# Kernel tuning notes

Measured on AMD Instinct MI355X. Metric: run time of the kernel, lower is better.

Reference implementation:

```python
import jax, jax.numpy as jnp
import numpy as np

K = 3
KK = K * K


def _offset_mask_conv(x, ow, ob):
    # Conv2d(C_in, 3*KK, k=3, stride=1, pad=1) in NCHW/OIHW
    y = jax.lax.conv_general_dilated(
        x, ow, window_strides=(1, 1), padding=((1, 1), (1, 1)),
        dimension_numbers=('NCHW', 'OIHW', 'NCHW'))
    return y + ob[None, :, None, None]


def _bilinear(xb, gy, gx):
    # xb: [C,H,W]; gy,gx: [KK,H,W] pixel coords (align_corners=True => pixel==unnormalized)
    # padding_mode='zeros': out-of-range taps contribute 0.
    C, H, W = xb.shape
    x0f = jnp.floor(gx); y0f = jnp.floor(gy)
    x0 = x0f.astype(jnp.int32); y0 = y0f.astype(jnp.int32)
    x1 = x0 + 1; y1 = y0 + 1
    wx1 = gx - x0f; wy1 = gy - y0f
    wx0 = 1.0 - wx1; wy0 = 1.0 - wy1

    def gather(yi, xi):
        valid = (yi >= 0) & (yi < H) & (xi >= 0) & (xi < W)
        yc = jnp.clip(yi, 0, H - 1)
        xc = jnp.clip(xi, 0, W - 1)
        v = xb[:, yc, xc]  # [C,KK,H,W]
        return v * valid[None].astype(xb.dtype)

    return (gather(y0, x0) * (wy0 * wx0)[None]
            + gather(y0, x1) * (wy0 * wx1)[None]
            + gather(y1, x0) * (wy1 * wx0)[None]
            + gather(y1, x1) * (wy1 * wx1)[None])  # [C,KK,H,W]


def setup_inputs() -> dict:
    key = jax.random.key(0)
    k1, k2, k3, k4 = jax.random.split(key, 4)
    B, C, Cout, H, W = 8, 64, 64, 128, 128
    x = jax.random.normal(k1, (B, C, H, W), dtype=jnp.float32)
    # offset/mask conv params (small, so offsets stay in a realistic range)
    ow = jax.random.normal(k2, (3 * KK, C, K, K), dtype=jnp.float32) * 0.01
    ob = jnp.zeros((3 * KK,), dtype=jnp.float32)
    # main conv weight (kaiming-ish scale) and bias
    w = jax.random.normal(k3, (Cout, C, K, K), dtype=jnp.float32) * (1.0 / np.sqrt(C * KK))
    b = jax.random.normal(k4, (Cout,), dtype=jnp.float32) * 0.01
    return {"x": x, "ow": ow, "ob": ob, "w": w, "b": b}


def reference(x, ow, ob, w, b):
    B, C, H, W = x.shape
    om = _offset_mask_conv(x, ow, ob)            # [B, 3*KK, H, W]
    off_x = om[:, :KK]                           # o1 -> x-offset
    off_y = om[:, KK:2 * KK]                     # o2 -> y-offset
    mask = jax.nn.sigmoid(om[:, 2 * KK:])        # [B,KK,H,W]

    gh, gw = jnp.meshgrid(jnp.arange(H, dtype=x.dtype), jnp.arange(W, dtype=x.dtype), indexing='ij')
    d = jnp.arange(-(K // 2), K // 2 + 1, dtype=x.dtype)
    kh, kw = jnp.meshgrid(d, d, indexing='ij')
    dh = kh.reshape(-1)                          # [KK] row-major (dh,dw) order matches weight[...,i,j]
    dw = kw.reshape(-1)

    gx = gw[None, None] + dw[None, :, None, None] + off_x   # [B,KK,H,W]
    gy = gh[None, None] + dh[None, :, None, None] + off_y

    sampled = jax.vmap(_bilinear)(x, gy, gx)     # [B,C,KK,H,W]
    sampled = sampled * mask[:, None]            # modulation

    wflat = w.reshape(w.shape[0], w.shape[1], KK)  # [Cout,C,KK]
    out = jnp.einsum('bckhw,ock->bohw', sampled, wflat) + b[None, :, None, None]
    return out
```

## Files before the change

### kernel.cpp

```cpp
#include <hip/hip_runtime.h>

#define B 8
#define C 64
#define H 128
#define W 128
#define HW (H * W)
#define OC 27
#define KK 9
#define COUT 64
#define KDIM 576
#define LDSROW 1152
#define NPIX 16
#define NPAIR (NPIX * KK)

typedef __attribute__((ext_vector_type(8))) short s16x8;
typedef __attribute__((ext_vector_type(4))) float f32x4;

__device__ inline ushort f2bf(float f) {
    union { float f; unsigned u; } uv;
    uv.f = f;
    unsigned r = uv.u + 0x7FFF + ((uv.u >> 16) & 1);
    return (ushort)(r >> 16);
}
__device__ inline float bf2f(ushort u) {
    return __uint_as_float((unsigned)u << 16);
}

__global__ __launch_bounds__(256) void k_transpose_x(const float* __restrict__ x,
                                                     ushort* __restrict__ xTb) {
    __shared__ float lds[64][65];
    int b = blockIdx.x >> 8;
    int tile = blockIdx.x & 255;
    int hw0 = tile * 64;
    int lane = threadIdx.x & 63;
    int cg = threadIdx.x >> 6;
#pragma unroll
    for (int r = 0; r < 16; ++r) {
        int c = cg * 16 + r;
        lds[c][lane] = x[(size_t)(b * C + c) * HW + hw0 + lane];
    }
    __syncthreads();
#pragma unroll
    for (int r = 0; r < 16; ++r) {
        int hwl = cg * 16 + r;
        xTb[(size_t)(b * HW + hw0 + hwl) * C + lane] = f2bf(lds[lane][hwl]);
    }
}

__global__ __launch_bounds__(256) void k_prep_w(const float* __restrict__ w,
                                                ushort* __restrict__ wB) {
    int idx = blockIdx.x * 256 + threadIdx.x;
    if (idx >= COUT * KDIM) return;
    int o = idx / KDIM;
    int Kx = idx % KDIM;
    int k = Kx >> 6;
    int c = Kx & 63;
    wB[idx] = f2bf(w[(size_t)(o * C + c) * KK + k]);
}

__global__ __launch_bounds__(256) void k_prep_aw(const float* __restrict__ ow,
                                                 ushort* __restrict__ awB) {
    int idx = blockIdx.x * 256 + threadIdx.x;
    if (idx >= 32 * KDIM) return;
    int o = idx / KDIM;
    int Kx = idx % KDIM;
    int tap = Kx >> 6;
    int c = Kx & 63;
    float v = (o < OC) ? ow[((size_t)o * C + c) * KK + tap] : 0.0f;
    awB[idx] = f2bf(v);
}

__global__ __launch_bounds__(256) void k_om(const ushort* __restrict__ xTb,
                                            const ushort* __restrict__ awB,
                                            const float* __restrict__ ob,
                                            float* __restrict__ om) {
    __shared__ __align__(16) char xwin[3 * 66 * 128];
    int tid = threadIdx.x;
    int lane = tid & 63;
    int wv = tid >> 6;
    int blk = blockIdx.x;
    int b = blk >> 8;
    int h = (blk >> 1) & 127;
    int w0 = (blk & 1) * 64;

    const ushort* xb = xTb + (size_t)b * (HW * C);
    int ch2 = tid & 31;
#pragma unroll
    for (int it = 0; it < 25; ++it) {
        int pi = it * 8 + (tid >> 5);
        if (pi < 198) {
            int row = pi / 66;
            int col = pi - row * 66;
            int y = h - 1 + row;
            int xc = w0 - 1 + col;
            unsigned v = 0;
            if ((unsigned)y < H && (unsigned)xc < W)
                v = *(const unsigned*)(xb + ((size_t)(y * W + xc) << 6) + ch2 * 2);
            int byte = (pi * 128 + ch2 * 4) ^ ((col & 7) << 4);
            *(unsigned*)(xwin + byte) = v;
        }
    }
    __syncthreads();

    f32x4 acc0 = {0.f, 0.f, 0.f, 0.f};
    f32x4 acc1 = {0.f, 0.f, 0.f, 0.f};
    int pixl = lane & 15;
    int q = lane >> 4;
    int base_col = wv * 16 + pixl;
    const ushort* a0 = awB + (size_t)pixl * KDIM + q * 8;
    const ushort* a1 = awB + (size_t)(16 + pixl) * KDIM + q * 8;
#pragma unroll
    for (int s = 0; s < 18; ++s) {
        int tap = s >> 1;
        int row = tap / 3;
        int cs = tap - row * 3;
        int col = base_col + cs;
        int c0b = ((s & 1) * 32 + q * 8) * 2;
        int byte = (((row * 66 + col) << 7) + c0b) ^ ((col & 7) << 4);
        s16x8 bfrag = *(const s16x8*)(xwin + byte);
        s16x8 af0 = *(const s16x8*)(a0 + s * 32);
        s16x8 af1 = *(const s16x8*)(a1 + s * 32);
        acc0 = __builtin_amdgcn_mfma_f32_16x16x32_bf16(af0, bfrag, acc0, 0, 0, 0);
        acc1 = __builtin_amdgcn_mfma_f32_16x16x32_bf16(af1, bfrag, acc1, 0, 0, 0);
    }

    int pix = wv * 16 + pixl;
#pragma unroll
    for (int j = 0; j < 4; ++j) {
        int oc = q * 4 + j;
        om[(((size_t)b * OC + oc) * H + h) * W + w0 + pix] = acc0[j] + ob[oc];
        int oc1 = 16 + q * 4 + j;
        if (oc1 < OC)
            om[(((size_t)b * OC + oc1) * H + h) * W + w0 + pix] = acc1[j] + ob[oc1];
    }
}

__global__ __launch_bounds__(256, 6) void k_main(const ushort* __restrict__ xTb,
                                                 const float* __restrict__ om,
                                                 const ushort* __restrict__ wB,
                                                 const float* __restrict__ bias,
                                                 float* __restrict__ out) {
    __shared__ __align__(16) char smem[NPIX * LDSROW];
    __shared__ float4 meta_w[NPAIR];
    __shared__ int2 meta_o[NPAIR];

    int tid = threadIdx.x;
    int lane = tid & 63;
    int wv = tid >> 6;
    int pb = blockIdx.x * NPIX;
    int b = pb >> 14;
    int rem = pb & (HW - 1);
    int h = rem >> 7;
    int w0 = rem & (W - 1);

    if (tid < NPAIR) {
        int k = tid >> 4;
        int p = tid & 15;
        int dh = k / 3 - 1;
        int dw = k % 3 - 1;
        const float* o0 = om + ((size_t)b * OC) * HW + h * W + w0 + p;
        float offx = o0[(size_t)k * HW];
        float offy = o0[(size_t)(KK + k) * HW];
        float mlog = o0[(size_t)(2 * KK + k) * HW];
        float mask = 1.0f / (1.0f + __expf(-mlog));
        float gx = (float)(w0 + p + dw) + offx;
        float gy = (float)(h + dh) + offy;
        float x0f = floorf(gx), y0f = floorf(gy);
        int x0 = (int)x0f, y0 = (int)y0f;
        int x1 = x0 + 1, y1 = y0 + 1;
        float wx1 = gx - x0f, wy1 = gy - y0f;
        float wx0 = 1.0f - wx1, wy0 = 1.0f - wy1;
        float rw0 = ((unsigned)y0 < H) ? wy0 * mask : 0.0f;
        float rw1 = ((unsigned)y1 < H) ? wy1 * mask : 0.0f;
        int y0c = min(max(y0, 0), H - 1), y1c = min(max(y1, 0), H - 1);
        int colbase = min(max(x0, 0), W - 2);
        float cw0 = 0.0f, cw1 = 0.0f;
        if ((unsigned)x0 < W) { if (x0 == colbase) cw0 += wx0; else cw1 += wx0; }
        if ((unsigned)x1 < W) { if (x1 == colbase) cw0 += wx1; else cw1 += wx1; }
        meta_w[tid] = make_float4(rw0 * cw0, rw0 * cw1, rw1 * cw0, rw1 * cw1);
        meta_o[tid] = make_int2((y0c * W + colbase) * (C * 2),
                                (y1c * W + colbase) * (C * 2));
    }
    __syncthreads();

    const char* xbase = (const char*)(xTb + (size_t)b * (HW * C));
#pragma unroll
    for (int pp = 0; pp < 4; ++pp) {
        int p = wv * 4 + pp;
        int vlds = p * LDSROW + ((lane * 2) ^ ((p & 7) << 4));
#pragma unroll
        for (int k = 0; k < KK; ++k) {
            int pair = k * 16 + p;
            float4 mw = meta_w[pair];
            int2 mo = meta_o[pair];
            const ushort* r0 =
                (const ushort*)(xbase + __builtin_amdgcn_readfirstlane(mo.x));
            const ushort* r1 =
                (const ushort*)(xbase + __builtin_amdgcn_readfirstlane(mo.y));
            float g00 = bf2f(r0[lane]);
            float g01 = bf2f(r0[64 + lane]);
            float g10 = bf2f(r1[lane]);
            float g11 = bf2f(r1[64 + lane]);
            float v = g00 * mw.x + g01 * mw.y + g10 * mw.z + g11 * mw.w;
            *(ushort*)(smem + vlds + k * 128) = f2bf(v);
        }
    }
    __syncthreads();

    f32x4 acc;
#pragma unroll
    for (int j = 0; j < 4; ++j) acc[j] = bias[wv * 16 + (lane >> 4) * 4 + j];

    int pix = lane & 15;
    const ushort* wrow = wB + (size_t)(wv * 16 + pix) * KDIM + (lane >> 4) * 8;
#pragma unroll
    for (int s = 0; s < 18; ++s) {
        int kbyte = s * 64 + (lane >> 4) * 16;
        int byte = (pix * LDSROW + kbyte) ^ ((pix & 7) << 4);
        s16x8 bfrag = *(const s16x8*)(smem + byte);
        s16x8 afrag = *(const s16x8*)(wrow + s * 32);
        acc = __builtin_amdgcn_mfma_f32_16x16x32_bf16(afrag, bfrag, acc, 0, 0, 0);
    }

    float* obase = out + ((size_t)(b * COUT + wv * 16 + (lane >> 4) * 4) * HW) + h * W + w0;
#pragma unroll
    for (int j = 0; j < 4; ++j) obase[(size_t)j * HW + pix] = acc[j];
}

extern "C" void kernel_launch(void* const* d_in, const int* in_sizes, int n_in,
                              void* d_out, int out_size, void* d_ws, size_t ws_size,
                              hipStream_t stream) {
    const float* x = (const float*)d_in[0];
    const float* ow = (const float*)d_in[1];
    const float* ob = (const float*)d_in[2];
    const float* w = (const float*)d_in[3];
    const float* bias = (const float*)d_in[4];
    float* out = (float*)d_out;

    float* om = (float*)d_ws;
    ushort* xTb = (ushort*)(om + (size_t)B * OC * HW);
    ushort* wB = xTb + (size_t)B * HW * C;
    ushort* awB = wB + (size_t)COUT * KDIM;

    hipLaunchKernelGGL(k_transpose_x, dim3(B * 256), dim3(256), 0, stream, x, xTb);
    hipLaunchKernelGGL(k_prep_w, dim3((COUT * KDIM + 255) / 256), dim3(256), 0,
                       stream, w, wB);
    hipLaunchKernelGGL(k_prep_aw, dim3((32 * KDIM + 255) / 256), dim3(256), 0,
                       stream, ow, awB);
    hipLaunchKernelGGL(k_om, dim3(B * H * 2), dim3(256), 0, stream, xTb, awB, ob, om);
    hipLaunchKernelGGL(k_main, dim3(B * HW / NPIX), dim3(256), 0, stream,
                       xTb, om, wB, bias, out);
}
```

Baseline: 172.0 us.

## Gather bilinear taps as packed bf16 pairs with cross-half shuffle reduction

The deformable sampling loop now loads 4-byte words (two bf16 channels) per lane instead of four separate 2-byte loads. The low half-wave handles the left column tap and the high half the right, and a 32-lane xor shuffle combines them. All 18 loads for a pixel are issued before any math to raise memory-level parallelism, and results are packed with the hardware bf16 convert. The aim is fewer, wider global loads and fewer instructions, at the cost of more registers, shuffle overhead, and half the lanes idling on the LDS store.

```diff
diff --git a/kernel.cpp b/kernel.cpp
--- a/kernel.cpp
+++ b/kernel.cpp
@@ -184,25 +184,37 @@
     __syncthreads();
 
     const char* xbase = (const char*)(xTb + (size_t)b * (HW * C));
+    bool lo_half = lane < 32;
 #pragma unroll
     for (int pp = 0; pp < 4; ++pp) {
         int p = wv * 4 + pp;
-        int vlds = p * LDSROW + ((lane * 2) ^ ((p & 7) << 4));
+        unsigned d0[KK], d1[KK];
+        float wa[KK], wb[KK];
 #pragma unroll
         for (int k = 0; k < KK; ++k) {
             int pair = k * 16 + p;
             float4 mw = meta_w[pair];
             int2 mo = meta_o[pair];
-            const ushort* r0 =
-                (const ushort*)(xbase + __builtin_amdgcn_readfirstlane(mo.x));
-            const ushort* r1 =
-                (const ushort*)(xbase + __builtin_amdgcn_readfirstlane(mo.y));
-            float g00 = bf2f(r0[lane]);
-            float g01 = bf2f(r0[64 + lane]);
-            float g10 = bf2f(r1[lane]);
-            float g11 = bf2f(r1[64 + lane]);
-            float v = g00 * mw.x + g01 * mw.y + g10 * mw.z + g11 * mw.w;
-            *(ushort*)(smem + vlds + k * 128) = f2bf(v);
+            wa[k] = lo_half ? mw.x : mw.y;
+            wb[k] = lo_half ? mw.z : mw.w;
+            d0[k] = *(const unsigned*)(xbase + mo.x + lane * 4);
+            d1[k] = *(const unsigned*)(xbase + mo.y + lane * 4);
+        }
+        int vlds = p * LDSROW + (((lane & 31) * 4) ^ ((p & 7) << 4));
+#pragma unroll
+        for (int k = 0; k < KK; ++k) {
+            float a0 = __uint_as_float(d0[k] << 16);
+            float a1 = __uint_as_float(d0[k] & 0xFFFF0000u);
+            float b0 = __uint_as_float(d1[k] << 16);
+            float b1 = __uint_as_float(d1[k] & 0xFFFF0000u);
+            float p0 = a0 * wa[k] + b0 * wb[k];
+            float p1 = a1 * wa[k] + b1 * wb[k];
+            float q0 = __shfl_xor(p0, 32, 64);
+            float q1 = __shfl_xor(p1, 32, 64);
+            float s0 = p0 + q0, s1 = p1 + q1;
+            unsigned pk;
+            asm("v_cvt_pk_bf16_f32 %0, %1, %2" : "=v"(pk) : "v"(s0), "v"(s1));
+            if (lane < 32) *(unsigned*)(smem + vlds + k * 128) = pk;
         }
     }
     __syncthreads();
```

Result: no change. 170.4 us (-1.0%).
